# Optimization experiments

Measured on AMD Instinct MI355X. Metric: run time of the kernel, lower is better.

The kernel has to match this reference:

```python
import jax, jax.numpy as jnp
import numpy as np

HIDDEN = 1024
TYPE_SIZE = 1000
BATCH = 32
SEQLEN = 512


def setup_inputs() -> dict:
    key = jax.random.key(0)
    k1, k2, k3, k4, k5 = jax.random.split(key, 5)
    event_seqs = jax.random.randint(k1, (BATCH, SEQLEN), 0, TYPE_SIZE + 1)
    duration_seqs = jax.random.uniform(k2, (BATCH, SEQLEN), dtype=jnp.float32)
    # nn.Linear(2H, 7H): weight [7H, 2H], bias [7H]
    bound = 1.0 / np.sqrt(2 * HIDDEN)
    W_rec = jax.random.uniform(k3, (7 * HIDDEN, 2 * HIDDEN), minval=-bound, maxval=bound, dtype=jnp.float32)
    b_rec = jax.random.uniform(k4, (7 * HIDDEN,), minval=-bound, maxval=bound, dtype=jnp.float32)
    emb_table = jax.random.normal(k5, (TYPE_SIZE + 1, HIDDEN), dtype=jnp.float32)
    return {"event_seqs": event_seqs, "duration_seqs": duration_seqs,
            "emb_table": emb_table, "W_rec": W_rec, "b_rec": b_rec}


def _ctlstm_forward(event_seqs, duration_seqs, emb_table, W_rec, b_rec):
    # batch_first=True: transpose to [T, B]
    ev = event_seqs.T          # [T, B]
    dur = duration_seqs.T      # [T, B]
    H = emb_table.shape[1]
    x = emb_table[ev]          # [T, B, H]
    # NOTE: the original forward re-inits h_d/c_d/c_bar to zeros every timestep,
    # so feed = concat(emb_t, zeros) and c_tm1 = c_bar_tm1 = 0: fully parallel in T.
    # rec(feed) with zero h-half == x @ W_rec[:, :H].T + b_rec
    gates = jnp.einsum('tbh,gh->tbg', x, W_rec[:, :H]) + b_rec  # [T, B, 7H]
    gi, gf, gz, go, gib, gfb, gd = jnp.split(gates, 7, axis=-1)
    gi = jax.nn.sigmoid(gi)
    gz = jnp.tanh(gz)
    go = jax.nn.sigmoid(go)
    gib = jax.nn.sigmoid(gib)
    gd = jax.nn.softplus(gd)
    # c_tm1 = 0, c_bar_tm1 = 0
    c = gi * gz                # [T, B, H]
    c_bar = gib * gz           # [T, B, H]
    c_d = c_bar + (c - c_bar) * jnp.exp(-gd * dur[..., None])
    h_d = go * jnp.tanh(c_d)
    return jnp.stack((h_d, c, c_bar, go, gd))  # [5, T, B, H]


def reference(event_seqs, duration_seqs, emb_table, W_rec, b_rec):
    return _ctlstm_forward(event_seqs, duration_seqs, emb_table, W_rec, b_rec)
```

## Files before the change

kernel.cpp:

```cpp
#include <hip/hip_runtime.h>
#include <stdint.h>

#define HID    1024
#define TYPES  1001
#define MPAD   1024
#define NGATES 5120
#define BATCH  32
#define SEQLEN 512
#define TB     (BATCH * SEQLEN)
#define TBH    ((size_t)TB * HID)
#define GSTRIDE ((size_t)MPAD * HID)

typedef __attribute__((ext_vector_type(4))) float  f32x4;
typedef __attribute__((ext_vector_type(8))) __bf16 bf16x8;

__device__ __forceinline__ uint32_t f2bf(float f) {
    uint32_t u = __float_as_uint(f);
    return (u + 0x7FFFu + ((u >> 16) & 1u)) >> 16;
}

__device__ __forceinline__ int gate_off(int g) {
    return (g + (g >= 1) + (g >= 4)) << 10;
}

#define GLD16(gp, lp) __builtin_amdgcn_global_load_lds(                        \
    (const __attribute__((address_space(1))) void*)(uintptr_t)(gp),            \
    (__attribute__((address_space(3))) void*)(uint32_t)(uintptr_t)(lp),        \
    16, 0, 0)

__global__ __launch_bounds__(256) void convert_kernel(
    const float* __restrict__ emb, const float* __restrict__ Wrec,
    uint16_t* __restrict__ Ebf, uint16_t* __restrict__ Wbf)
{
    const int row = blockIdx.x;
    const int tid = threadIdx.x;
    const float* src;
    uint16_t* dst;
    if (row < TYPES) {
        src = emb + (size_t)row * HID;
        dst = Ebf + (size_t)row * HID;
    } else {
        const int n = row - TYPES;
        const int g = n >> 10;
        const int h = n & 1023;
        src = Wrec + (size_t)(gate_off(g) + h) * (2 * HID);
        dst = Wbf + (size_t)n * HID;
    }
    float4 v = ((const float4*)src)[tid];
    uint2 p;
    p.x = f2bf(v.x) | (f2bf(v.y) << 16);
    p.y = f2bf(v.z) | (f2bf(v.w) << 16);
    ((uint2*)dst)[tid] = p;
}

__global__ __launch_bounds__(256) void gemm_gates(
    const uint16_t* __restrict__ E, const uint16_t* __restrict__ W,
    const float* __restrict__ brec, float* __restrict__ G)
{
    __shared__ uint16_t As[128 * 32];
    __shared__ uint16_t Bs[128 * 32];
    const int tM = blockIdx.x;
    const int tN = blockIdx.y;
    const int t = threadIdx.x;
    const int wave = t >> 6;
    const int lane = t & 63;
    const int lane15 = lane & 15;
    const int quad = lane >> 4;
    const int m0 = (wave >> 1) * 64;
    const int n0 = (wave & 1) * 64;

    f32x4 acc[4][4] = {};

    const uint16_t* Ag = E + (size_t)(tM * 128 + (t >> 2)) * HID + (t & 3) * 8;
    const uint16_t* Bg = W + (size_t)(tN * 128 + (t >> 2)) * HID + (t & 3) * 8;
    uint16_t* Al = &As[(t >> 2) * 32 + (t & 3) * 8];
    uint16_t* Bl = &Bs[(t >> 2) * 32 + (t & 3) * 8];

    for (int k0 = 0; k0 < HID; k0 += 32) {
        GLD16(Ag + k0, Al);
        GLD16(Ag + k0 + (size_t)64 * HID, Al + 64 * 32);
        GLD16(Bg + k0, Bl);
        GLD16(Bg + k0 + (size_t)64 * HID, Bl + 64 * 32);
        __syncthreads();

        bf16x8 af[4], bfr[4];
        #pragma unroll
        for (int i = 0; i < 4; i++)
            af[i] = *(const bf16x8*)&As[(m0 + i * 16 + lane15) * 32 + quad * 8];
        #pragma unroll
        for (int i = 0; i < 4; i++)
            bfr[i] = *(const bf16x8*)&Bs[(n0 + i * 16 + lane15) * 32 + quad * 8];

        #pragma unroll
        for (int im = 0; im < 4; im++)
            #pragma unroll
            for (int in = 0; in < 4; in++)
                acc[im][in] = __builtin_amdgcn_mfma_f32_16x16x32_bf16(
                    af[im], bfr[in], acc[im][in], 0, 0, 0);
        __syncthreads();
    }

    #pragma unroll
    for (int in = 0; in < 4; in++) {
        const int n = tN * 128 + n0 + in * 16 + lane15;
        const int g = n >> 10;
        const int h = n & 1023;
        const float bias = brec[gate_off(g) + h];
        float* Gg = G + (size_t)g * GSTRIDE + h;
        #pragma unroll
        for (int im = 0; im < 4; im++) {
            const int mb = tM * 128 + m0 + im * 16 + quad * 4;
            #pragma unroll
            for (int r = 0; r < 4; r++) {
                const float v = acc[im][in][r] + bias;
                float o;
                if (g == 1) {
                    float e = __expf(2.f * v);
                    o = 1.f - 2.f / (e + 1.f);
                } else if (g == 4) {
                    o = fmaxf(v, 0.f) + log1pf(__expf(-fabsf(v)));
                } else {
                    o = 1.f / (1.f + __expf(-v));
                }
                Gg[(size_t)(mb + r) * HID] = o;
            }
        }
    }
}

__global__ __launch_bounds__(256) void expand_kernel(
    const int* __restrict__ ev, const float* __restrict__ dur,
    const float* __restrict__ G, float* __restrict__ out)
{
    const int tb = blockIdx.x;
    const int t = tb >> 5;
    const int b = tb & 31;
    const int src = b * SEQLEN + t;
    const int u = ev[src];
    const float d = dur[src];
    const int tid = threadIdx.x;

    const float* Gu = G + (size_t)u * HID;
    f32x4 gi  = *((const f32x4*)(Gu + 0 * GSTRIDE) + tid);
    f32x4 gz  = *((const f32x4*)(Gu + 1 * GSTRIDE) + tid);
    f32x4 go  = *((const f32x4*)(Gu + 2 * GSTRIDE) + tid);
    f32x4 gib = *((const f32x4*)(Gu + 3 * GSTRIDE) + tid);
    f32x4 gd  = *((const f32x4*)(Gu + 4 * GSTRIDE) + tid);

    f32x4 c, cb, hd;
    #pragma unroll
    for (int j = 0; j < 4; j++) {
        float ci  = gi[j] * gz[j];
        float cbi = gib[j] * gz[j];
        float e   = __expf(-gd[j] * d);
        float cdi = cbi + (ci - cbi) * e;
        float t2  = __expf(2.f * cdi);
        c[j]  = ci;
        cb[j] = cbi;
        hd[j] = go[j] * (1.f - 2.f / (t2 + 1.f));
    }

    float* o = out + (size_t)tb * HID;
    __builtin_nontemporal_store(hd, (f32x4*)(o + 0 * TBH) + tid);
    __builtin_nontemporal_store(c,  (f32x4*)(o + 1 * TBH) + tid);
    __builtin_nontemporal_store(cb, (f32x4*)(o + 2 * TBH) + tid);
    __builtin_nontemporal_store(go, (f32x4*)(o + 3 * TBH) + tid);
    __builtin_nontemporal_store(gd, (f32x4*)(o + 4 * TBH) + tid);
}

extern "C" void kernel_launch(void* const* d_in, const int* in_sizes, int n_in,
                              void* d_out, int out_size, void* d_ws, size_t ws_size,
                              hipStream_t stream) {
    const int*   ev   = (const int*)d_in[0];
    const float* dur  = (const float*)d_in[1];
    const float* emb  = (const float*)d_in[2];
    const float* Wrec = (const float*)d_in[3];
    const float* brec = (const float*)d_in[4];
    float* out = (float*)d_out;

    char* ws = (char*)d_ws;
    uint16_t* Ebf = (uint16_t*)ws;
    uint16_t* Wbf = (uint16_t*)(ws + (size_t)2 * 1024 * 1024);
    float*    G   = (float*)(ws + (size_t)12 * 1024 * 1024);

    convert_kernel<<<dim3(TYPES + NGATES), dim3(256), 0, stream>>>(emb, Wrec, Ebf, Wbf);
    gemm_gates<<<dim3(8, 40), dim3(256), 0, stream>>>(Ebf, Wbf, brec, G);
    expand_kernel<<<dim3(TB), dim3(256), 0, stream>>>(ev, dur, G, out);
}
```

Baseline: 448.4 us.

## Double-buffer GEMM LDS tiles and interleave gate table rows per token

The gate GEMM now uses two LDS buffers per operand, so the next K-tile's global-to-LDS load is issued before the current tile's MFMAs run, and the trailing barrier is dropped. The gate table G is also re-laid out so all five gates for one token type sit contiguously (5*HID floats per row), making the expand kernel's five gathered loads hit one contiguous 20KB region. The cost is double the shared memory per block. The GEMM's scattered strided stores change pattern as well.

Result: no change. 449.9 us (+0.3%).

```diff
diff --git a/kernel.cpp b/kernel.cpp
--- a/kernel.cpp
+++ b/kernel.cpp
@@ -9,7 +9,7 @@
 #define SEQLEN 512
 #define TB     (BATCH * SEQLEN)
 #define TBH    ((size_t)TB * HID)
-#define GSTRIDE ((size_t)MPAD * HID)
+#define GROW   (5 * HID)
 
 typedef __attribute__((ext_vector_type(4))) float  f32x4;
 typedef __attribute__((ext_vector_type(8))) __bf16 bf16x8;
@@ -57,8 +57,8 @@
     const uint16_t* __restrict__ E, const uint16_t* __restrict__ W,
     const float* __restrict__ brec, float* __restrict__ G)
 {
-    __shared__ uint16_t As[128 * 32];
-    __shared__ uint16_t Bs[128 * 32];
+    __shared__ uint16_t As[2 * 128 * 32];
+    __shared__ uint16_t Bs[2 * 128 * 32];
     const int tM = blockIdx.x;
     const int tN = blockIdx.y;
     const int t = threadIdx.x;
@@ -76,20 +76,32 @@
     uint16_t* Al = &As[(t >> 2) * 32 + (t & 3) * 8];
     uint16_t* Bl = &Bs[(t >> 2) * 32 + (t & 3) * 8];
 
-    for (int k0 = 0; k0 < HID; k0 += 32) {
-        GLD16(Ag + k0, Al);
-        GLD16(Ag + k0 + (size_t)64 * HID, Al + 64 * 32);
-        GLD16(Bg + k0, Bl);
-        GLD16(Bg + k0 + (size_t)64 * HID, Bl + 64 * 32);
+    GLD16(Ag, Al);
+    GLD16(Ag + (size_t)64 * HID, Al + 64 * 32);
+    GLD16(Bg, Bl);
+    GLD16(Bg + (size_t)64 * HID, Bl + 64 * 32);
+
+    int cur = 0;
+    for (int kt = 0; kt < 32; ++kt) {
         __syncthreads();
-
+        const int knext = (kt + 1) * 32;
+        const int nxt = cur ^ 1;
+        if (knext < HID) {
+            GLD16(Ag + knext, Al + (nxt << 12));
+            GLD16(Ag + knext + (size_t)64 * HID, Al + (nxt << 12) + 64 * 32);
+            GLD16(Bg + knext, Bl + (nxt << 12));
+            GLD16(Bg + knext + (size_t)64 * HID, Bl + (nxt << 12) + 64 * 32);
+        }
+
+        const uint16_t* Asc = As + (cur << 12);
+        const uint16_t* Bsc = Bs + (cur << 12);
         bf16x8 af[4], bfr[4];
         #pragma unroll
         for (int i = 0; i < 4; i++)
-            af[i] = *(const bf16x8*)&As[(m0 + i * 16 + lane15) * 32 + quad * 8];
+            af[i] = *(const bf16x8*)&Asc[(m0 + i * 16 + lane15) * 32 + quad * 8];
         #pragma unroll
         for (int i = 0; i < 4; i++)
-            bfr[i] = *(const bf16x8*)&Bs[(n0 + i * 16 + lane15) * 32 + quad * 8];
+            bfr[i] = *(const bf16x8*)&Bsc[(n0 + i * 16 + lane15) * 32 + quad * 8];
 
         #pragma unroll
         for (int im = 0; im < 4; im++)
@@ -97,7 +109,7 @@
             for (int in = 0; in < 4; in++)
                 acc[im][in] = __builtin_amdgcn_mfma_f32_16x16x32_bf16(
                     af[im], bfr[in], acc[im][in], 0, 0, 0);
-        __syncthreads();
+        cur = nxt;
     }
 
     #pragma unroll
@@ -106,7 +118,6 @@
         const int g = n >> 10;
         const int h = n & 1023;
         const float bias = brec[gate_off(g) + h];
-        float* Gg = G + (size_t)g * GSTRIDE + h;
         #pragma unroll
         for (int im = 0; im < 4; im++) {
             const int mb = tM * 128 + m0 + im * 16 + quad * 4;
@@ -122,7 +133,7 @@
                 } else {
                     o = 1.f / (1.f + __expf(-v));
                 }
-                Gg[(size_t)(mb + r) * HID] = o;
+                G[((size_t)(mb + r) * 5 + g) * HID + h] = o;
             }
         }
     }
@@ -140,12 +151,12 @@
     const float d = dur[src];
     const int tid = threadIdx.x;
 
-    const float* Gu = G + (size_t)u * HID;
-    f32x4 gi  = *((const f32x4*)(Gu + 0 * GSTRIDE) + tid);
-    f32x4 gz  = *((const f32x4*)(Gu + 1 * GSTRIDE) + tid);
-    f32x4 go  = *((const f32x4*)(Gu + 2 * GSTRIDE) + tid);
-    f32x4 gib = *((const f32x4*)(Gu + 3 * GSTRIDE) + tid);
-    f32x4 gd  = *((const f32x4*)(Gu + 4 * GSTRIDE) + tid);
+    const f32x4* Gu = (const f32x4*)(G + (size_t)u * GROW);
+    f32x4 gi  = Gu[0 * 256 + tid];
+    f32x4 gz  = Gu[1 * 256 + tid];
+    f32x4 go  = Gu[2 * 256 + tid];
+    f32x4 gib = Gu[3 * 256 + tid];
+    f32x4 gd  = Gu[4 * 256 + tid];
 
     f32x4 c, cb, hd;
     #pragma unroll
```
